# Performance work log

Measured on AMD Instinct MI355X. Metric: run time of the kernel, lower is better.

## Reference

```python
import jax, jax.numpy as jnp
import numpy as np
import math

B_, L_, D_, N_ = 8, 2048, 1024, 64


def _ln(x, g, b):
    m = jnp.mean(x, axis=-1, keepdims=True)
    v = jnp.mean((x - m) ** 2, axis=-1, keepdims=True)
    return (x - m) / jnp.sqrt(v + 1e-5) * g + b


def _ssm_kernel(A, Bp, Cp, Dp, L):
    # diagonal SSM: lambda = exp(diag(A)); k[l] = C diag(lambda)^l B + D  -> shape (L,)
    a = jnp.diagonal(A)                                   # (N,)
    powers = jnp.exp(jnp.arange(L)[:, None] * a[None, :])  # (L, N) = lambda^l
    return powers @ (Bp[:, 0] * Cp[0]) + Dp[0]             # (L,)


def _causal_conv(h, k):
    # y[:, t, :] = sum_{j<=t} k[j] * h[:, t-j, :]  via zero-padded FFT (same math, O(L log L))
    L = h.shape[1]
    n = 2 * L
    Hf = jnp.fft.rfft(h, n=n, axis=1)
    Kf = jnp.fft.rfft(k, n=n)
    return jnp.fft.irfft(Hf * Kf[None, :, None], n=n, axis=1)[:, :L]


def _timestep_embedding(t, dim):
    half = dim // 2
    freqs = jnp.exp(jnp.arange(half) * (-math.log(10000.0) / (half - 1)))
    ang = t[:, None] * freqs[None, :]
    return jnp.concatenate([jnp.sin(ang), jnp.cos(ang)], axis=1)  # (B, dim)


def _conv1d(x, w, b):
    # x: (B, C, L), w: (O, I, 3) torch layout, padding=1
    y = jax.lax.conv_general_dilated(x, w, (1,), [(1, 1)],
                                     dimension_numbers=('NCH', 'OIH', 'NCH'))
    return y + b[None, :, None]


def setup_inputs():
    key = jax.random.key(0)
    ks = jax.random.split(key, 26)
    d = {}
    d['x'] = jax.random.normal(ks[0], (B_, L_, D_), jnp.float32)
    d['t'] = jax.random.uniform(ks[1], (B_,), jnp.float32) * 1000.0
    d['beta1'] = jax.random.uniform(ks[2], (1,), jnp.float32)
    d['beta2'] = jax.random.uniform(ks[3], (1,), jnp.float32)
    sc = 1.0 / math.sqrt(D_)
    d['Wi'] = jax.random.normal(ks[4], (D_, D_), jnp.float32) * sc
    d['bi'] = jnp.zeros((D_,), jnp.float32)
    d['Wo'] = jax.random.normal(ks[5], (D_, D_), jnp.float32) * sc
    d['bo'] = jnp.zeros((D_,), jnp.float32)
    d['w1'] = jax.random.normal(ks[6], (D_, D_, 3), jnp.float32) * 0.02
    d['bc1'] = jnp.zeros((D_,), jnp.float32)
    d['w2'] = jax.random.normal(ks[7], (D_, D_, 3), jnp.float32) * 0.02
    d['bc2'] = jnp.zeros((D_,), jnp.float32)
    d['g1'] = jnp.ones((D_,), jnp.float32)
    d['b1'] = jnp.zeros((D_,), jnp.float32)
    d['g2'] = jnp.ones((D_,), jnp.float32)
    d['b2'] = jnp.zeros((D_,), jnp.float32)
    # SSM params (std 0.001 on A keeps exp(l*a) bounded for l up to L)
    d['Af'] = jax.random.normal(ks[8], (N_, N_), jnp.float32) * 0.001
    d['Bf'] = jax.random.normal(ks[9], (N_, 1), jnp.float32) * 0.01
    d['Cf'] = jax.random.normal(ks[10], (1, N_), jnp.float32) * 0.01
    d['Df'] = jax.random.normal(ks[11], (1,), jnp.float32) * 0.01
    d['Ab'] = jax.random.normal(ks[12], (N_, N_), jnp.float32) * 0.001
    d['Bb'] = jax.random.normal(ks[13], (N_, 1), jnp.float32) * 0.01
    d['Cb'] = jax.random.normal(ks[14], (1, N_), jnp.float32) * 0.01
    d['Db'] = jax.random.normal(ks[15], (1,), jnp.float32) * 0.01
    return d


def reference(x, t, beta1, beta2, Wi, bi, Wo, bo, w1, bc1, w2, bc2,
              g1, b1, g2, b2, Af, Bf, Cf, Df, Ab, Bb, Cb, Db):
    Bsz, L, D = x.shape
    h = x @ Wi + bi
    h = _ln(h, g1, b1)
    # local conv branch
    hT = jnp.transpose(h, (0, 2, 1))                 # (B, D, L)
    co = jax.nn.silu(_conv1d(hT, w1, bc1))
    co = _conv1d(co, w2, bc2)
    conv_out = jnp.transpose(co, (0, 2, 1))          # (B, L, D)
    # bidirectional SSM global convolutions
    kf = _ssm_kernel(Af, Bf, Cf, Df, L)
    h_fwd = _causal_conv(h, kf)
    kb = _ssm_kernel(Ab, Bb, Cb, Db, L)
    h_bwd = jnp.flip(_causal_conv(jnp.flip(h, axis=1), kb), axis=1)
    # timestep-conditioned mixing
    noise_scale = jax.nn.sigmoid(_timestep_embedding(t, D))[:, None, :]  # (B,1,D)
    h = h_fwd * (beta1[0] * noise_scale) + h_bwd * (beta2[0] * noise_scale) + conv_out
    h = h @ Wo + bo
    h = _ln(h, g2, b2)
    return x + h
```

## Files before the change

kernel.cpp:

```cpp
#include <hip/hip_runtime.h>

#define Bq 8
#define Lq 2048
#define Dq 1024
#define LPq 2050

typedef unsigned short u16;
typedef __attribute__((ext_vector_type(8))) short bf16x8;
typedef __attribute__((ext_vector_type(4))) float f32x4;

__device__ __forceinline__ u16 f2bf(float f) {
  unsigned u = __float_as_uint(f);
  u += 0x7FFFu + ((u >> 16) & 1u);
  return (u16)(u >> 16);
}
__device__ __forceinline__ float bf2f(u16 s) {
  return __uint_as_float(((unsigned)s) << 16);
}
__device__ __forceinline__ void gld16(const u16* g, u16* l) {
  __builtin_amdgcn_global_load_lds((const __attribute__((address_space(1))) void*)g,
                                   (__attribute__((address_space(3))) void*)l, 16, 0, 0);
}


__global__ __launch_bounds__(256) void prep_small(
    const float* __restrict__ t,
    const float* __restrict__ Af, const float* __restrict__ Bf, const float* __restrict__ Cf, const float* __restrict__ Df,
    const float* __restrict__ Ab, const float* __restrict__ Bb, const float* __restrict__ Cb, const float* __restrict__ Db,
    float* __restrict__ kf, float* __restrict__ kb,
    float* __restrict__ ns,
    u16* __restrict__ hpad, u16* __restrict__ copad) {
  int tid = blockIdx.x * 256 + threadIdx.x;
  if (blockIdx.x < 8) {
    int l = tid;
    float sf = Df[0], sb = Db[0];
    for (int n = 0; n < 64; n++) {
      sf += __expf((float)l * Af[n * 64 + n]) * (Bf[n] * Cf[n]);
      sb += __expf((float)l * Ab[n * 64 + n]) * (Bb[n] * Cb[n]);
    }
    kf[l] = sf; kb[l] = sb;
  } else if (blockIdx.x < 40) {
    int i = tid - 2048;
    int b = i >> 10, d = i & 1023;
    float tb = t[b];
    float e;
    if (d < 512) {
      float f = __expf((float)d * (-logf(10000.f) / 511.f));
      e = sinf(tb * f);
    } else {
      float f = __expf((float)(d - 512) * (-logf(10000.f) / 511.f));
      e = cosf(tb * f);
    }
    ns[i] = 1.f / (1.f + __expf(-e));
  } else {
    int i = tid - 10240;
    if (i < 32768) {
      int d = i & 1023;
      int j = i >> 10;
      int arr = j & 1, r = (j >> 1) & 1, b = j >> 2;
      size_t off = (size_t)b * LPq * Dq + (r ? (size_t)(LPq - 1) * Dq : 0) + d;
      if (arr == 0) hpad[off] = 0;
      else          copad[off] = 0;
    }
  }
}

__global__ __launch_bounds__(256) void mega_prep(
    const float* __restrict__ x, u16* __restrict__ xb,
    const float* __restrict__ Wi, u16* __restrict__ wit,
    const float* __restrict__ Wo, u16* __restrict__ wot,
    const float* __restrict__ w1, u16* __restrict__ w1t,
    const float* __restrict__ w2, u16* __restrict__ w2t,
    const float* __restrict__ kf, const float* __restrict__ kb,
    const float* __restrict__ be1, const float* __restrict__ be2,
    u16* __restrict__ Tm) {
  int bid = blockIdx.x, tid = threadIdx.x;
  if (bid < 8192) {
    size_t i = ((size_t)bid * 256 + tid) * 8;
    float4 a = *(const float4*)(x + i);
    float4 b = *(const float4*)(x + i + 4);
    u16 o[8] = {f2bf(a.x), f2bf(a.y), f2bf(a.z), f2bf(a.w),
                f2bf(b.x), f2bf(b.y), f2bf(b.z), f2bf(b.w)};
    *(bf16x8*)(xb + i) = *(const bf16x8*)o;
  } else if (bid < 8704) {
    __shared__ float tile[64][65];
    const float* W = (bid < 8448) ? Wi : Wo;
    u16* Wt = (bid < 8448) ? wit : wot;
    int b2 = (bid < 8448) ? bid - 8192 : bid - 8448;
    int bx = b2 & 15, by = b2 >> 4;
    int tx = tid & 63, tw = tid >> 6;
    for (int r = tw; r < 64; r += 4)
      tile[r][tx] = W[(size_t)(by * 64 + r) * 1024 + bx * 64 + tx];
    __syncthreads();
    for (int r = tw; r < 64; r += 4)
      Wt[(size_t)(bx * 64 + r) * 1024 + by * 64 + tx] = f2bf(tile[tx][r]);
  } else if (bid < 14848) {
    const float* w = (bid < 11776) ? w1 : w2;
    u16* Wt = (bid < 11776) ? w1t : w2t;
    int vb = (bid < 11776) ? bid - 8704 : bid - 11776;
    int base = (vb * 256 + tid) * 4;
    int o = base / 3072, rem = base % 3072;
    int dt = rem >> 10, i0 = rem & 1023;
    const float* src = w + (size_t)o * 3072 + dt;
    ushort4 v;
    v.x = f2bf(src[(i0 + 0) * 3]);
    v.y = f2bf(src[(i0 + 1) * 3]);
    v.z = f2bf(src[(i0 + 2) * 3]);
    v.w = f2bf(src[(i0 + 3) * 3]);
    *(ushort4*)(Wt + base) = v;
  } else {
    int idx = (bid - 14848) * 256 + tid;
    int tr = idx >> 9, j0 = (idx & 511) * 4;
    float b1v = be1[0], b2v = be2[0];
    ushort4 v;
#pragma unroll
    for (int q = 0; q < 4; q++) {
      int j = j0 + q;
      float vv = 0.f;
      if (tr >= j) vv += b1v * kf[tr - j];
      if (j >= tr) vv += b2v * kb[j - tr];
      ((u16*)&v)[q] = f2bf(vv);
    }
    *(ushort4*)(Tm + (size_t)tr * 2048 + j0) = v;
  }
}

__global__ __launch_bounds__(256) void trans_h(const u16* __restrict__ hpad, u16* __restrict__ ht) {
  __shared__ u16 tile[64][66];
  int b = blockIdx.z;
  int lt = blockIdx.x * 64, dt = blockIdx.y * 64;
  int tx = threadIdx.x & 15, ty = threadIdx.x >> 4;
  const u16* src = hpad + (size_t)b * LPq * Dq + (size_t)(lt + 1 + ty) * Dq + dt + tx * 4;
#pragma unroll
  for (int i = 0; i < 4; i++) {
    int r = ty + i * 16;
    ushort4 v = *(const ushort4*)(src + (size_t)i * 16 * Dq);
    tile[tx * 4 + 0][r] = v.x;
    tile[tx * 4 + 1][r] = v.y;
    tile[tx * 4 + 2][r] = v.z;
    tile[tx * 4 + 3][r] = v.w;
  }
  __syncthreads();
#pragma unroll
  for (int i = 0; i < 4; i++) {
    int d = ty + i * 16;
    ushort4 v;
    v.x = tile[d][tx * 4 + 0];
    v.y = tile[d][tx * 4 + 1];
    v.z = tile[d][tx * 4 + 2];
    v.w = tile[d][tx * 4 + 3];
    *(ushort4*)(ht + ((size_t)b * Dq + dt + d) * Lq + lt + tx * 4) = v;
  }
}


__global__ __launch_bounds__(256) void ln1_k(const u16* __restrict__ h0, u16* __restrict__ hpad,
                                             const float* __restrict__ g, const float* __restrict__ be) {
  int w = threadIdx.x >> 6, lane = threadIdx.x & 63;
  int r = blockIdx.x * 4 + w;
  int d0 = lane * 16;
  const u16* hp = h0 + (size_t)r * 1024 + d0;
  bf16x8 va = *(const bf16x8*)hp;
  bf16x8 vb = *(const bf16x8*)(hp + 8);
  float v[16];
#pragma unroll
  for (int i = 0; i < 8; i++) { v[i] = bf2f((u16)va[i]); v[8 + i] = bf2f((u16)vb[i]); }
  float s = 0.f, q = 0.f;
#pragma unroll
  for (int i = 0; i < 16; i++) { s += v[i]; q += v[i] * v[i]; }
#pragma unroll
  for (int o = 32; o > 0; o >>= 1) { s += __shfl_xor(s, o); q += __shfl_xor(q, o); }
  float mean = s * (1.f / 1024.f);
  float rstd = rsqrtf(q * (1.f / 1024.f) - mean * mean + 1e-5f);
  const float4* g4 = (const float4*)(g + d0);
  const float4* b4 = (const float4*)(be + d0);
  u16 o16[16];
#pragma unroll
  for (int i = 0; i < 4; i++) {
    float4 gv = g4[i], bv = b4[i];
    o16[i * 4 + 0] = f2bf((v[i * 4 + 0] - mean) * rstd * gv.x + bv.x);
    o16[i * 4 + 1] = f2bf((v[i * 4 + 1] - mean) * rstd * gv.y + bv.y);
    o16[i * 4 + 2] = f2bf((v[i * 4 + 2] - mean) * rstd * gv.z + bv.z);
    o16[i * 4 + 3] = f2bf((v[i * 4 + 3] - mean) * rstd * gv.w + bv.w);
  }
  int b_ = r >> 11, l = r & 2047;
  u16* dst = hpad + ((size_t)b_ * LPq + l + 1) * Dq + d0;
  *(bf16x8*)dst = *(const bf16x8*)o16;
  *(bf16x8*)(dst + 8) = *(const bf16x8*)(o16 + 8);
}

__global__ __launch_bounds__(256) void ln2_k(const u16* __restrict__ hp, const float* __restrict__ x,
                                             const float* __restrict__ g, const float* __restrict__ be,
                                             float* __restrict__ out) {
  int w = threadIdx.x >> 6, lane = threadIdx.x & 63;
  size_t r = (size_t)blockIdx.x * 4 + w;
  int d0 = lane * 16;
  size_t base = r * 1024 + d0;
  const u16* h = hp + base;
  bf16x8 va = *(const bf16x8*)h;
  bf16x8 vb = *(const bf16x8*)(h + 8);
  float v[16];
#pragma unroll
  for (int i = 0; i < 8; i++) { v[i] = bf2f((u16)va[i]); v[8 + i] = bf2f((u16)vb[i]); }
  float s = 0.f, q = 0.f;
#pragma unroll
  for (int i = 0; i < 16; i++) { s += v[i]; q += v[i] * v[i]; }
#pragma unroll
  for (int o = 32; o > 0; o >>= 1) { s += __shfl_xor(s, o); q += __shfl_xor(q, o); }
  float mean = s * (1.f / 1024.f);
  float rstd = rsqrtf(q * (1.f / 1024.f) - mean * mean + 1e-5f);
  const float4* g4 = (const float4*)(g + d0);
  const float4* b4 = (const float4*)(be + d0);
  const float4* x4 = (const float4*)(x + base);
  float4* o4 = (float4*)(out + base);
#pragma unroll
  for (int i = 0; i < 4; i++) {
    float4 gv = g4[i], bv = b4[i], xv = x4[i];
    float4 o;
    o.x = xv.x + (v[i * 4 + 0] - mean) * rstd * gv.x + bv.x;
    o.y = xv.y + (v[i * 4 + 1] - mean) * rstd * gv.y + bv.y;
    o.z = xv.z + (v[i * 4 + 2] - mean) * rstd * gv.z + bv.z;
    o.w = xv.w + (v[i * 4 + 3] - mean) * rstd * gv.w + bv.w;
    o4[i] = o;
  }
}

__device__ __forceinline__ void gemm_core(const u16* __restrict__ Ab, int lda,
                                          const u16* __restrict__ Bb, int ldb,
                                          int ks, int NS, u16* lds,
                                          f32x4 (&acc)[8][4]) {
  const int t = threadIdx.x;
  const int lane = t & 63, w = t >> 6;
  const int g = w >> 2, j = w & 3;
  const int p1 = t >> 3;
  const int c1 = (t & 7) ^ (p1 & 7);
  const int row1 = (p1 << 1) | (c1 >> 2), f1 = c1 & 3;
  const int q2 = t + 512;
  const int p2 = q2 >> 3;
  const int c2 = (q2 & 7) ^ (p2 & 7);
  const int row2 = (p2 << 1) | (c2 >> 2), f2 = c2 & 3;
  const int aoff1 = row1 * lda + f1 * 8;
  const int aoff2 = row2 * lda + f2 * 8;
  const int boff1 = row1 * ldb + f1 * 8;
  const int boff2 = row2 * ldb + f2 * 8;
  u16* wA1 = lds + t * 8;
  u16* wA2 = lds + 4096 + t * 8;
  u16* wB1 = lds + 8192 + t * 8;
  u16* wB2 = lds + 12288 + t * 8;
  const int frow = lane & 15, fkc = lane >> 4;
  const int arow = g * 128 + frow;
  const int pa = arow >> 1, ca = ((arow & 1) << 2) | fkc;
  const int abase = pa * 64 + ((ca ^ (pa & 7)) << 3);
  const int brow = j * 64 + frow;
  const int pb = brow >> 1, cb = ((brow & 1) << 2) | fkc;
  const int bbase = 8192 + pb * 64 + ((cb ^ (pb & 7)) << 3);

#define STAGE_A(s_) { int sl_ = ((s_) & 3) * 16384; const u16* g_ = Ab + ks + (s_) * 32; \
    gld16(g_ + aoff1, wA1 + sl_); gld16(g_ + aoff2, wA2 + sl_); }
#define STAGE_B(s_) { int sl_ = ((s_) & 3) * 16384; const u16* g_ = Bb + ks + (s_) * 32; \
    gld16(g_ + boff1, wB1 + sl_); gld16(g_ + boff2, wB2 + sl_); }

  STAGE_A(0); STAGE_B(0);
  STAGE_A(1); STAGE_B(1);
  STAGE_A(2); STAGE_B(2);

  for (int s = 0; s < NS; s++) {
    const u16* sl = lds + (s & 3) * 16384;
    if (s <= NS - 3)      { asm volatile("s_waitcnt vmcnt(8)" ::: "memory"); }
    else if (s == NS - 2) { asm volatile("s_waitcnt vmcnt(4)" ::: "memory"); }
    else                  { asm volatile("s_waitcnt vmcnt(0)" ::: "memory"); }
    asm volatile("s_barrier" ::: "memory");
    if (s + 3 < NS) STAGE_A(s + 3);
    bf16x8 bq[4], af[4];
#pragma unroll
    for (int nf = 0; nf < 4; nf++) bq[nf] = *(const bf16x8*)(sl + bbase + nf * 512);
#pragma unroll
    for (int mf = 0; mf < 4; mf++) af[mf] = *(const bf16x8*)(sl + abase + mf * 512);
    __builtin_amdgcn_s_setprio(1);
#pragma unroll
    for (int mf = 0; mf < 4; mf++)
#pragma unroll
      for (int nf = 0; nf < 4; nf++)
        acc[mf][nf] = __builtin_amdgcn_mfma_f32_16x16x32_bf16(af[mf], bq[nf], acc[mf][nf], 0, 0, 0);
    __builtin_amdgcn_s_setprio(0);
    if (s + 3 < NS) STAGE_B(s + 3);
#pragma unroll
    for (int mf = 0; mf < 4; mf++) af[mf] = *(const bf16x8*)(sl + abase + 2048 + mf * 512);
    __builtin_amdgcn_s_setprio(1);
#pragma unroll
    for (int mf = 0; mf < 4; mf++)
#pragma unroll
      for (int nf = 0; nf < 4; nf++)
        acc[4 + mf][nf] = __builtin_amdgcn_mfma_f32_16x16x32_bf16(af[mf], bq[nf], acc[4 + mf][nf], 0, 0, 0);
    __builtin_amdgcn_s_setprio(0);
  }
#undef STAGE_A
#undef STAGE_B
}

template <int MODE>
__global__ __launch_bounds__(512, 2) void gemm8(
    const u16* __restrict__ A, int lda, long abstr,
    const u16* __restrict__ Bw, int ldb,
    u16* __restrict__ Out, long obstr,
    const float* __restrict__ bias, int K, int nbm) {
  __shared__ __align__(16) u16 lds[65536];
  int mb = blockIdx.x % nbm, nb = blockIdx.x / nbm;
  int m0 = mb * 256, n0 = nb * 256;
  int batch = m0 >> 11, r0 = m0 & 2047;
  const u16* Ab = A + (size_t)batch * abstr + (size_t)r0 * lda;
  const u16* Bb = Bw + (size_t)n0 * ldb;
  f32x4 acc[8][4] = {};
  gemm_core(Ab, lda, Bb, ldb, 0, K >> 5, lds, acc);
  int lane = threadIdx.x & 63, w = threadIdx.x >> 6;
  int g = w >> 2, j = w & 3;
  int frow = lane & 15;
  u16* ob = Out + (size_t)batch * obstr;
#pragma unroll
  for (int mf = 0; mf < 8; mf++) {
    int row = r0 + g * 128 + mf * 16 + ((lane >> 4) << 2);
#pragma unroll
    for (int nf = 0; nf < 4; nf++) {
      int col = n0 + j * 64 + nf * 16 + frow;
      float bv = bias[col];
      size_t base = (size_t)row * 1024 + col;
      f32x4 a = acc[mf][nf];
#pragma unroll
      for (int i = 0; i < 4; i++) {
        float v = a[i] + bv;
        if (MODE == 1) v = v / (1.f + __expf(-v));
        if (MODE == 2) v += bf2f(ob[base + (size_t)i * 1024]);
        ob[base + (size_t)i * 1024] = f2bf(v);
      }
    }
  }
}

__global__ __launch_bounds__(512, 2) void ssm8(
    const u16* __restrict__ Tm, const u16* __restrict__ Ht,
    const float* __restrict__ ns, u16* __restrict__ out) {
  __shared__ __align__(16) u16 lds[65536];
  int mb = blockIdx.x & 7, nb = blockIdx.x >> 3;
  int m0 = mb * 256, n0 = nb * 256;
  const u16* Ab = Tm + (size_t)m0 * 2048;
  const u16* Bb = Ht + (size_t)n0 * 2048;
  f32x4 acc[8][4] = {};
  gemm_core(Ab, 2048, Bb, 2048, 0, 64, lds, acc);
  int lane = threadIdx.x & 63, w = threadIdx.x >> 6;
  int g = w >> 2, j = w & 3;
  int frow = lane & 15;
#pragma unroll
  for (int mf = 0; mf < 8; mf++) {
    int row = m0 + g * 128 + mf * 16 + ((lane >> 4) << 2);
#pragma unroll
    for (int nf = 0; nf < 4; nf++) {
      int col = n0 + j * 64 + nf * 16 + frow;
      int b = col >> 10, d = col & 1023;
      float cv = ns[col];
      u16* op = out + ((size_t)b * Lq + row) * 1024 + d;
      f32x4 a = acc[mf][nf];
#pragma unroll
      for (int i = 0; i < 4; i++)
        op[(size_t)i * 1024] = f2bf(a[i] * cv);
    }
  }
}


extern "C" void kernel_launch(void* const* d_in, const int* in_sizes, int n_in,
                              void* d_out, int out_size, void* d_ws, size_t ws_size,
                              hipStream_t stream) {
  const float* x   = (const float*)d_in[0];
  const float* tt  = (const float*)d_in[1];
  const float* be1 = (const float*)d_in[2];
  const float* be2 = (const float*)d_in[3];
  const float* Wi  = (const float*)d_in[4];
  const float* bi  = (const float*)d_in[5];
  const float* Wo  = (const float*)d_in[6];
  const float* bo  = (const float*)d_in[7];
  const float* w1  = (const float*)d_in[8];
  const float* bc1 = (const float*)d_in[9];
  const float* w2  = (const float*)d_in[10];
  const float* bc2 = (const float*)d_in[11];
  const float* g1  = (const float*)d_in[12];
  const float* b1  = (const float*)d_in[13];
  const float* g2  = (const float*)d_in[14];
  const float* b2  = (const float*)d_in[15];
  const float* Af  = (const float*)d_in[16];
  const float* Bf  = (const float*)d_in[17];
  const float* Cf  = (const float*)d_in[18];
  const float* Df  = (const float*)d_in[19];
  const float* Ab  = (const float*)d_in[20];
  const float* Bb  = (const float*)d_in[21];
  const float* Cb  = (const float*)d_in[22];
  const float* Db  = (const float*)d_in[23];

  char* p = (char*)d_ws;
  constexpr size_t SZ_h0   = (size_t)16384 * 1024 * 2;
  constexpr size_t SZ_hpad = (size_t)Bq * LPq * Dq * 2;
  constexpr size_t SZ_ht   = (size_t)Bq * Dq * Lq * 2;
  constexpr size_t SZ_hmix = (size_t)16384 * 1024 * 2;
  constexpr size_t SZ_T    = (size_t)2048 * 2048 * 2;
  constexpr size_t SZ_wt   = (size_t)1024 * 1024 * 2;
  constexpr size_t SZ_w3t  = (size_t)1024 * 3072 * 2;

  size_t off = 0;
  u16* h0    = (u16*)(p + off); off += SZ_h0;
  u16* hpad  = (u16*)(p + off); off += SZ_hpad;
  u16* ht    = (u16*)(p + off); off += SZ_ht;
  u16* copad = (u16*)(p + off); off += SZ_hpad;
  u16* hmixF = (u16*)(p + off); off += SZ_hmix;
  u16* Tmat  = (u16*)(p + off); off += SZ_T;
  u16* wit   = (u16*)(p + off); off += SZ_wt;
  u16* wot   = (u16*)(p + off); off += SZ_wt;
  u16* w1t   = (u16*)(p + off); off += SZ_w3t;
  u16* w2t   = (u16*)(p + off); off += SZ_w3t;
  float* kf  = (float*)(p + off); off += 8192;
  float* kb  = (float*)(p + off); off += 8192;
  float* nsb = (float*)(p + off); off += 32768;
  u16* xb    = hmixF;

  const long BSTR = (long)2048 * 1024;
  const long PSTR = (long)LPq * 1024;

  prep_small<<<dim3(168), dim3(256), 0, stream>>>(tt, Af, Bf, Cf, Df,
                                                  Ab, Bb, Cb, Db, kf, kb, nsb, hpad, copad);
  mega_prep<<<dim3(18944), dim3(256), 0, stream>>>(x, xb, Wi, wit, Wo, wot,
                                                   w1, w1t, w2, w2t, kf, kb, be1, be2, Tmat);

  gemm8<0><<<dim3(256), dim3(512), 0, stream>>>(xb, 1024, BSTR, wit, 1024, h0, BSTR, bi, 1024, 64);
  ln1_k<<<dim3(4096), dim3(256), 0, stream>>>(h0, hpad, g1, b1);
  trans_h<<<dim3(32, 16, 8), dim3(256), 0, stream>>>(hpad, ht);
  gemm8<1><<<dim3(256), dim3(512), 0, stream>>>(hpad, 1024, PSTR, w1t, 3072, copad + 1024, PSTR, bc1, 3072, 64);
  ssm8<<<dim3(256), dim3(512), 0, stream>>>(Tmat, ht, nsb, hmixF);
  gemm8<2><<<dim3(256), dim3(512), 0, stream>>>(copad, 1024, PSTR, w2t, 3072, hmixF, BSTR, bc2, 3072, 64);
  gemm8<0><<<dim3(256), dim3(512), 0, stream>>>(hmixF, 1024, BSTR, wot, 1024, h0, BSTR, bo, 1024, 64);
  ln2_k<<<dim3(4096), dim3(256), 0, stream>>>(h0, x, g2, b2, (float*)d_out);
}
```

Baseline: 446.6 us.

## Switch GEMM core to 32x32x16 MFMA and merge conv1 and SSM GEMMs into one launch

The shared GEMM core now uses 32x32x16 bf16 MFMA tiles instead of 16x16x32. That means fewer instructions and fewer LDS fragment reads per unit of output, with the LDS addressing and epilogue row/column mapping rewritten to match. The conv1 GEMM (with SiLU) and the SSM Toeplitz GEMM are independent, so they are fused into a single 512-block kernel. This lets both fill the GPU together and removes one launch and its tail. The cost is an epilogue layout that must match the 32x32 accumulator ordering, and register use stays the same.

After: 478.0 us. +7.0%, slower.

```diff
diff --git a/kernel.cpp b/kernel.cpp
--- a/kernel.cpp
+++ b/kernel.cpp
@@ -7,7 +7,7 @@
 
 typedef unsigned short u16;
 typedef __attribute__((ext_vector_type(8))) short bf16x8;
-typedef __attribute__((ext_vector_type(4))) float f32x4;
+typedef __attribute__((ext_vector_type(16))) float f32x16;
 
 __device__ __forceinline__ u16 f2bf(float f) {
   unsigned u = __float_as_uint(f);
@@ -228,7 +228,7 @@
 __device__ __forceinline__ void gemm_core(const u16* __restrict__ Ab, int lda,
                                           const u16* __restrict__ Bb, int ldb,
                                           int ks, int NS, u16* lds,
-                                          f32x4 (&acc)[8][4]) {
+                                          f32x16 (&acc)[4][2]) {
   const int t = threadIdx.x;
   const int lane = t & 63, w = t >> 6;
   const int g = w >> 2, j = w & 3;
@@ -247,13 +247,24 @@
   u16* wA2 = lds + 4096 + t * 8;
   u16* wB1 = lds + 8192 + t * 8;
   u16* wB2 = lds + 12288 + t * 8;
-  const int frow = lane & 15, fkc = lane >> 4;
-  const int arow = g * 128 + frow;
-  const int pa = arow >> 1, ca = ((arow & 1) << 2) | fkc;
-  const int abase = pa * 64 + ((ca ^ (pa & 7)) << 3);
-  const int brow = j * 64 + frow;
-  const int pb = brow >> 1, cb = ((brow & 1) << 2) | fkc;
-  const int bbase = 8192 + pb * 64 + ((cb ^ (pb & 7)) << 3);
+  const int r32 = lane & 31, kh = lane >> 5;
+  int aadr[4][2], badr[2][2];
+#pragma unroll
+  for (int mf = 0; mf < 4; mf++)
+#pragma unroll
+    for (int kk = 0; kk < 2; kk++) {
+      int r = g * 128 + mf * 32 + r32;
+      int p = r >> 1, c = ((r & 1) << 2) | (kk * 2 + kh);
+      aadr[mf][kk] = p * 64 + ((c ^ (p & 7)) << 3);
+    }
+#pragma unroll
+  for (int nf = 0; nf < 2; nf++)
+#pragma unroll
+    for (int kk = 0; kk < 2; kk++) {
+      int r = j * 64 + nf * 32 + r32;
+      int p = r >> 1, c = ((r & 1) << 2) | (kk * 2 + kh);
+      badr[nf][kk] = 8192 + p * 64 + ((c ^ (p & 7)) << 3);
+    }
 
 #define STAGE_A(s_) { int sl_ = ((s_) & 3) * 16384; const u16* g_ = Ab + ks + (s_) * 32; \
     gld16(g_ + aoff1, wA1 + sl_); gld16(g_ + aoff2, wA2 + sl_); }
@@ -271,27 +282,30 @@
     else                  { asm volatile("s_waitcnt vmcnt(0)" ::: "memory"); }
     asm volatile("s_barrier" ::: "memory");
     if (s + 3 < NS) STAGE_A(s + 3);
-    bf16x8 bq[4], af[4];
-#pragma unroll
-    for (int nf = 0; nf < 4; nf++) bq[nf] = *(const bf16x8*)(sl + bbase + nf * 512);
-#pragma unroll
-    for (int mf = 0; mf < 4; mf++) af[mf] = *(const bf16x8*)(sl + abase + mf * 512);
+    bf16x8 b0[2], b1[2], a0[4], a1[4];
+#pragma unroll
+    for (int nf = 0; nf < 2; nf++) {
+      b0[nf] = *(const bf16x8*)(sl + badr[nf][0]);
+      b1[nf] = *(const bf16x8*)(sl + badr[nf][1]);
+    }
+#pragma unroll
+    for (int mf = 0; mf < 4; mf++) a0[mf] = *(const bf16x8*)(sl + aadr[mf][0]);
     __builtin_amdgcn_s_setprio(1);
 #pragma unroll
     for (int mf = 0; mf < 4; mf++)
 #pragma unroll
-      for (int nf = 0; nf < 4; nf++)
-        acc[mf][nf] = __builtin_amdgcn_mfma_f32_16x16x32_bf16(af[mf], bq[nf], acc[mf][nf], 0, 0, 0);
+      for (int nf = 0; nf < 2; nf++)
+        acc[mf][nf] = __builtin_amdgcn_mfma_f32_32x32x16_bf16(a0[mf], b0[nf], acc[mf][nf], 0, 0, 0);
     __builtin_amdgcn_s_setprio(0);
     if (s + 3 < NS) STAGE_B(s + 3);
 #pragma unroll
-    for (int mf = 0; mf < 4; mf++) af[mf] = *(const bf16x8*)(sl + abase + 2048 + mf * 512);
+    for (int mf = 0; mf < 4; mf++) a1[mf] = *(const bf16x8*)(sl + aadr[mf][1]);
     __builtin_amdgcn_s_setprio(1);
 #pragma unroll
     for (int mf = 0; mf < 4; mf++)
 #pragma unroll
-      for (int nf = 0; nf < 4; nf++)
-        acc[4 + mf][nf] = __builtin_amdgcn_mfma_f32_16x16x32_bf16(af[mf], bq[nf], acc[4 + mf][nf], 0, 0, 0);
+      for (int nf = 0; nf < 2; nf++)
+        acc[mf][nf] = __builtin_amdgcn_mfma_f32_32x32x16_bf16(a1[mf], b1[nf], acc[mf][nf], 0, 0, 0);
     __builtin_amdgcn_s_setprio(0);
   }
 #undef STAGE_A
@@ -310,58 +324,100 @@
   int batch = m0 >> 11, r0 = m0 & 2047;
   const u16* Ab = A + (size_t)batch * abstr + (size_t)r0 * lda;
   const u16* Bb = Bw + (size_t)n0 * ldb;
-  f32x4 acc[8][4] = {};
+  f32x16 acc[4][2] = {};
   gemm_core(Ab, lda, Bb, ldb, 0, K >> 5, lds, acc);
   int lane = threadIdx.x & 63, w = threadIdx.x >> 6;
   int g = w >> 2, j = w & 3;
-  int frow = lane & 15;
+  int r32 = lane & 31, kh = lane >> 5;
   u16* ob = Out + (size_t)batch * obstr;
 #pragma unroll
-  for (int mf = 0; mf < 8; mf++) {
-    int row = r0 + g * 128 + mf * 16 + ((lane >> 4) << 2);
-#pragma unroll
-    for (int nf = 0; nf < 4; nf++) {
-      int col = n0 + j * 64 + nf * 16 + frow;
+  for (int mf = 0; mf < 4; mf++) {
+#pragma unroll
+    for (int nf = 0; nf < 2; nf++) {
+      int col = n0 + j * 64 + nf * 32 + r32;
       float bv = bias[col];
-      size_t base = (size_t)row * 1024 + col;
-      f32x4 a = acc[mf][nf];
-#pragma unroll
-      for (int i = 0; i < 4; i++) {
-        float v = a[i] + bv;
-        if (MODE == 1) v = v / (1.f + __expf(-v));
-        if (MODE == 2) v += bf2f(ob[base + (size_t)i * 1024]);
-        ob[base + (size_t)i * 1024] = f2bf(v);
+      f32x16 a = acc[mf][nf];
+#pragma unroll
+      for (int q = 0; q < 4; q++) {
+        int row = r0 + g * 128 + mf * 32 + q * 8 + 4 * kh;
+        u16* op = ob + (size_t)row * 1024 + col;
+#pragma unroll
+        for (int i = 0; i < 4; i++) {
+          float v = a[q * 4 + i] + bv;
+          if (MODE == 1) v = v / (1.f + __expf(-v));
+          if (MODE == 2) v += bf2f(op[(size_t)i * 1024]);
+          op[(size_t)i * 1024] = f2bf(v);
+        }
       }
     }
   }
 }
 
-__global__ __launch_bounds__(512, 2) void ssm8(
+__global__ __launch_bounds__(512, 2) void mix8(
+    const u16* __restrict__ hpad, const u16* __restrict__ w1t,
+    u16* __restrict__ co, const float* __restrict__ bc1,
     const u16* __restrict__ Tm, const u16* __restrict__ Ht,
-    const float* __restrict__ ns, u16* __restrict__ out) {
+    const float* __restrict__ ns, u16* __restrict__ hmix) {
   __shared__ __align__(16) u16 lds[65536];
-  int mb = blockIdx.x & 7, nb = blockIdx.x >> 3;
-  int m0 = mb * 256, n0 = nb * 256;
-  const u16* Ab = Tm + (size_t)m0 * 2048;
-  const u16* Bb = Ht + (size_t)n0 * 2048;
-  f32x4 acc[8][4] = {};
-  gemm_core(Ab, 2048, Bb, 2048, 0, 64, lds, acc);
+  const long PSTR = (long)LPq * 1024;
+  int id = blockIdx.x;
   int lane = threadIdx.x & 63, w = threadIdx.x >> 6;
   int g = w >> 2, j = w & 3;
-  int frow = lane & 15;
-#pragma unroll
-  for (int mf = 0; mf < 8; mf++) {
-    int row = m0 + g * 128 + mf * 16 + ((lane >> 4) << 2);
-#pragma unroll
-    for (int nf = 0; nf < 4; nf++) {
-      int col = n0 + j * 64 + nf * 16 + frow;
-      int b = col >> 10, d = col & 1023;
-      float cv = ns[col];
-      u16* op = out + ((size_t)b * Lq + row) * 1024 + d;
-      f32x4 a = acc[mf][nf];
-#pragma unroll
-      for (int i = 0; i < 4; i++)
-        op[(size_t)i * 1024] = f2bf(a[i] * cv);
+  int r32 = lane & 31, kh = lane >> 5;
+  if (id < 256) {
+    int mb = id & 63, nb = id >> 6;
+    int m0 = mb * 256, n0 = nb * 256;
+    int batch = m0 >> 11, r0 = m0 & 2047;
+    const u16* Ab = hpad + (size_t)batch * PSTR + (size_t)r0 * 1024;
+    const u16* Bb = w1t + (size_t)n0 * 3072;
+    f32x16 acc[4][2] = {};
+    gemm_core(Ab, 1024, Bb, 3072, 0, 96, lds, acc);
+    u16* ob = co + (size_t)batch * PSTR;
+#pragma unroll
+    for (int mf = 0; mf < 4; mf++) {
+#pragma unroll
+      for (int nf = 0; nf < 2; nf++) {
+        int col = n0 + j * 64 + nf * 32 + r32;
+        float bv = bc1[col];
+        f32x16 a = acc[mf][nf];
+#pragma unroll
+        for (int q = 0; q < 4; q++) {
+          int row = r0 + g * 128 + mf * 32 + q * 8 + 4 * kh;
+          u16* op = ob + (size_t)row * 1024 + col;
+#pragma unroll
+          for (int i = 0; i < 4; i++) {
+            float v = a[q * 4 + i] + bv;
+            v = v / (1.f + __expf(-v));
+            op[(size_t)i * 1024] = f2bf(v);
+          }
+        }
+      }
+    }
+  } else {
+    int r = id - 256;
+    int mb = r & 7, nb = r >> 3;
+    int m0 = mb * 256, n0 = nb * 256;
+    const u16* Ab = Tm + (size_t)m0 * 2048;
+    const u16* Bb = Ht + (size_t)n0 * 2048;
+    f32x16 acc[4][2] = {};
+    gemm_core(Ab, 2048, Bb, 2048, 0, 64, lds, acc);
+#pragma unroll
+    for (int mf = 0; mf < 4; mf++) {
+#pragma unroll
+      for (int nf = 0; nf < 2; nf++) {
+        int col = n0 + j * 64 + nf * 32 + r32;
+        int b = col >> 10, d = col & 1023;
+        float cv = ns[col];
+        f32x16 a = acc[mf][nf];
+#pragma unroll
+        for (int q = 0; q < 4; q++) {
+          int row = m0 + g * 128 + mf * 32 + q * 8 + 4 * kh;
+          u16* op = hmix + ((size_t)b * Lq + row) * 1024 + d;
+#pragma unroll
+          for (int i = 0; i < 4; i++)
+            op[(size_t)i * 1024] = f2bf(a[q * 4 + i] * cv);
+        }
+      }
     }
   }
 }
@@ -431,8 +487,8 @@
   gemm8<0><<<dim3(256), dim3(512), 0, stream>>>(xb, 1024, BSTR, wit, 1024, h0, BSTR, bi, 1024, 64);
   ln1_k<<<dim3(4096), dim3(256), 0, stream>>>(h0, hpad, g1, b1);
   trans_h<<<dim3(32, 16, 8), dim3(256), 0, stream>>>(hpad, ht);
-  gemm8<1><<<dim3(256), dim3(512), 0, stream>>>(hpad, 1024, PSTR, w1t, 3072, copad + 1024, PSTR, bc1, 3072, 64);
-  ssm8<<<dim3(256), dim3(512), 0, stream>>>(Tmat, ht, nsb, hmixF);
+  mix8<<<dim3(512), dim3(512), 0, stream>>>(hpad, w1t, copad + 1024, bc1,
+                                            Tmat, ht, nsb, hmixF);
   gemm8<2><<<dim3(256), dim3(512), 0, stream>>>(copad, 1024, PSTR, w2t, 3072, hmixF, BSTR, bc2, 3072, 64);
   gemm8<0><<<dim3(256), dim3(512), 0, stream>>>(hmixF, 1024, BSTR, wot, 1024, h0, BSTR, bo, 1024, 64);
   ln2_k<<<dim3(4096), dim3(256), 0, stream>>>(h0, x, g2, b2, (float*)d_out);
```

## Use K=64 double-buffered GEMM tiles and merge conv1 and SSM GEMMs into one launch

Applied to the files above, without the earlier changes.

The GEMM core now stages 64-wide K slices into two LDS buffers instead of 32-wide slices into a four-deep ring, so each stage issues four async loads per operand and waits on vmcnt(0) before the barrier. The first conv GEMM and the SSM Toeplitz GEMM, which are independent, are merged into a single 512-block launch. This lowers launch overhead and fills the GPU with both workloads at once. The cost is a shallower prefetch pipeline (one stage ahead with a full wait), which may expose more memory latency.

Result: faster. 407.3 us (-8.8%).

```diff
diff --git a/kernel.cpp b/kernel.cpp
--- a/kernel.cpp
+++ b/kernel.cpp
@@ -227,55 +227,52 @@
 
 __device__ __forceinline__ void gemm_core(const u16* __restrict__ Ab, int lda,
                                           const u16* __restrict__ Bb, int ldb,
-                                          int ks, int NS, u16* lds,
+                                          int NS, u16* lds,
                                           f32x4 (&acc)[8][4]) {
   const int t = threadIdx.x;
   const int lane = t & 63, w = t >> 6;
   const int g = w >> 2, j = w & 3;
-  const int p1 = t >> 3;
-  const int c1 = (t & 7) ^ (p1 & 7);
-  const int row1 = (p1 << 1) | (c1 >> 2), f1 = c1 & 3;
-  const int q2 = t + 512;
-  const int p2 = q2 >> 3;
-  const int c2 = (q2 & 7) ^ (p2 & 7);
-  const int row2 = (p2 << 1) | (c2 >> 2), f2 = c2 & 3;
-  const int aoff1 = row1 * lda + f1 * 8;
-  const int aoff2 = row2 * lda + f2 * 8;
-  const int boff1 = row1 * ldb + f1 * 8;
-  const int boff2 = row2 * ldb + f2 * 8;
-  u16* wA1 = lds + t * 8;
-  u16* wA2 = lds + 4096 + t * 8;
-  u16* wB1 = lds + 8192 + t * 8;
-  u16* wB2 = lds + 12288 + t * 8;
-  const int frow = lane & 15, fkc = lane >> 4;
-  const int arow = g * 128 + frow;
-  const int pa = arow >> 1, ca = ((arow & 1) << 2) | fkc;
-  const int abase = pa * 64 + ((ca ^ (pa & 7)) << 3);
-  const int brow = j * 64 + frow;
-  const int pb = brow >> 1, cb = ((brow & 1) << 2) | fkc;
-  const int bbase = 8192 + pb * 64 + ((cb ^ (pb & 7)) << 3);
-
-#define STAGE_A(s_) { int sl_ = ((s_) & 3) * 16384; const u16* g_ = Ab + ks + (s_) * 32; \
-    gld16(g_ + aoff1, wA1 + sl_); gld16(g_ + aoff2, wA2 + sl_); }
-#define STAGE_B(s_) { int sl_ = ((s_) & 3) * 16384; const u16* g_ = Bb + ks + (s_) * 32; \
-    gld16(g_ + boff1, wB1 + sl_); gld16(g_ + boff2, wB2 + sl_); }
+  int aoff[4], boff[4];
+#pragma unroll
+  for (int q = 0; q < 4; q++) {
+    int c = t + q * 512;
+    int row = c >> 3;
+    int slot = (c & 7) ^ (row & 7);
+    aoff[q] = row * lda + slot * 8;
+    boff[q] = row * ldb + slot * 8;
+  }
+  const int frow = lane & 15, f = lane >> 4;
+  int aadr[8], badr[4];
+#pragma unroll
+  for (int mf = 0; mf < 8; mf++) {
+    int row = g * 128 + mf * 16 + frow;
+    aadr[mf] = row * 64 + ((f ^ (row & 7)) << 3);
+  }
+#pragma unroll
+  for (int nf = 0; nf < 4; nf++) {
+    int row = j * 64 + nf * 16 + frow;
+    badr[nf] = 16384 + row * 64 + ((f ^ (row & 7)) << 3);
+  }
+
+#define STAGE_A(s_) { const u16* g_ = Ab + (s_) * 64; u16* l_ = lds + ((s_) & 1) * 32768; \
+    gld16(g_ + aoff[0], l_ + t * 8);            gld16(g_ + aoff[1], l_ + (t + 512) * 8); \
+    gld16(g_ + aoff[2], l_ + (t + 1024) * 8);   gld16(g_ + aoff[3], l_ + (t + 1536) * 8); }
+#define STAGE_B(s_) { const u16* g_ = Bb + (s_) * 64; u16* l_ = lds + ((s_) & 1) * 32768 + 16384; \
+    gld16(g_ + boff[0], l_ + t * 8);            gld16(g_ + boff[1], l_ + (t + 512) * 8); \
+    gld16(g_ + boff[2], l_ + (t + 1024) * 8);   gld16(g_ + boff[3], l_ + (t + 1536) * 8); }
 
   STAGE_A(0); STAGE_B(0);
-  STAGE_A(1); STAGE_B(1);
-  STAGE_A(2); STAGE_B(2);
 
   for (int s = 0; s < NS; s++) {
-    const u16* sl = lds + (s & 3) * 16384;
-    if (s <= NS - 3)      { asm volatile("s_waitcnt vmcnt(8)" ::: "memory"); }
-    else if (s == NS - 2) { asm volatile("s_waitcnt vmcnt(4)" ::: "memory"); }
-    else                  { asm volatile("s_waitcnt vmcnt(0)" ::: "memory"); }
+    const u16* sl = lds + (s & 1) * 32768;
+    asm volatile("s_waitcnt vmcnt(0)" ::: "memory");
     asm volatile("s_barrier" ::: "memory");
-    if (s + 3 < NS) STAGE_A(s + 3);
+    if (s + 1 < NS) STAGE_A(s + 1);
     bf16x8 bq[4], af[4];
 #pragma unroll
-    for (int nf = 0; nf < 4; nf++) bq[nf] = *(const bf16x8*)(sl + bbase + nf * 512);
-#pragma unroll
-    for (int mf = 0; mf < 4; mf++) af[mf] = *(const bf16x8*)(sl + abase + mf * 512);
+    for (int nf = 0; nf < 4; nf++) bq[nf] = *(const bf16x8*)(sl + badr[nf]);
+#pragma unroll
+    for (int mf = 0; mf < 4; mf++) af[mf] = *(const bf16x8*)(sl + aadr[mf]);
     __builtin_amdgcn_s_setprio(1);
 #pragma unroll
     for (int mf = 0; mf < 4; mf++)
@@ -283,9 +280,29 @@
       for (int nf = 0; nf < 4; nf++)
         acc[mf][nf] = __builtin_amdgcn_mfma_f32_16x16x32_bf16(af[mf], bq[nf], acc[mf][nf], 0, 0, 0);
     __builtin_amdgcn_s_setprio(0);
-    if (s + 3 < NS) STAGE_B(s + 3);
-#pragma unroll
-    for (int mf = 0; mf < 4; mf++) af[mf] = *(const bf16x8*)(sl + abase + 2048 + mf * 512);
+    if (s + 1 < NS) STAGE_B(s + 1);
+#pragma unroll
+    for (int mf = 0; mf < 4; mf++) af[mf] = *(const bf16x8*)(sl + aadr[4 + mf]);
+    __builtin_amdgcn_s_setprio(1);
+#pragma unroll
+    for (int mf = 0; mf < 4; mf++)
+#pragma unroll
+      for (int nf = 0; nf < 4; nf++)
+        acc[4 + mf][nf] = __builtin_amdgcn_mfma_f32_16x16x32_bf16(af[mf], bq[nf], acc[4 + mf][nf], 0, 0, 0);
+    __builtin_amdgcn_s_setprio(0);
+#pragma unroll
+    for (int nf = 0; nf < 4; nf++) bq[nf] = *(const bf16x8*)(sl + (badr[nf] ^ 32));
+#pragma unroll
+    for (int mf = 0; mf < 4; mf++) af[mf] = *(const bf16x8*)(sl + (aadr[mf] ^ 32));
+    __builtin_amdgcn_s_setprio(1);
+#pragma unroll
+    for (int mf = 0; mf < 4; mf++)
+#pragma unroll
+      for (int nf = 0; nf < 4; nf++)
+        acc[mf][nf] = __builtin_amdgcn_mfma_f32_16x16x32_bf16(af[mf], bq[nf], acc[mf][nf], 0, 0, 0);
+    __builtin_amdgcn_s_setprio(0);
+#pragma unroll
+    for (int mf = 0; mf < 4; mf++) af[mf] = *(const bf16x8*)(sl + (aadr[4 + mf] ^ 32));
     __builtin_amdgcn_s_setprio(1);
 #pragma unroll
     for (int mf = 0; mf < 4; mf++)
@@ -311,7 +328,7 @@
   const u16* Ab = A + (size_t)batch * abstr + (size_t)r0 * lda;
   const u16* Bb = Bw + (size_t)n0 * ldb;
   f32x4 acc[8][4] = {};
-  gemm_core(Ab, lda, Bb, ldb, 0, K >> 5, lds, acc);
+  gemm_core(Ab, lda, Bb, ldb, K >> 6, lds, acc);
   int lane = threadIdx.x & 63, w = threadIdx.x >> 6;
   int g = w >> 2, j = w & 3;
   int frow = lane & 15;
@@ -336,32 +353,65 @@
   }
 }
 
-__global__ __launch_bounds__(512, 2) void ssm8(
+__global__ __launch_bounds__(512, 2) void mix8(
+    const u16* __restrict__ hpad, const u16* __restrict__ w1t,
+    u16* __restrict__ co, const float* __restrict__ bc1,
     const u16* __restrict__ Tm, const u16* __restrict__ Ht,
-    const float* __restrict__ ns, u16* __restrict__ out) {
+    const float* __restrict__ ns, u16* __restrict__ hmix) {
   __shared__ __align__(16) u16 lds[65536];
-  int mb = blockIdx.x & 7, nb = blockIdx.x >> 3;
-  int m0 = mb * 256, n0 = nb * 256;
-  const u16* Ab = Tm + (size_t)m0 * 2048;
-  const u16* Bb = Ht + (size_t)n0 * 2048;
-  f32x4 acc[8][4] = {};
-  gemm_core(Ab, 2048, Bb, 2048, 0, 64, lds, acc);
+  const long PSTR = (long)LPq * 1024;
+  int id = blockIdx.x;
   int lane = threadIdx.x & 63, w = threadIdx.x >> 6;
   int g = w >> 2, j = w & 3;
   int frow = lane & 15;
-#pragma unroll
-  for (int mf = 0; mf < 8; mf++) {
-    int row = m0 + g * 128 + mf * 16 + ((lane >> 4) << 2);
-#pragma unroll
-    for (int nf = 0; nf < 4; nf++) {
-      int col = n0 + j * 64 + nf * 16 + frow;
-      int b = col >> 10, d = col & 1023;
-      float cv = ns[col];
-      u16* op = out + ((size_t)b * Lq + row) * 1024 + d;
-      f32x4 a = acc[mf][nf];
-#pragma unroll
-      for (int i = 0; i < 4; i++)
-        op[(size_t)i * 1024] = f2bf(a[i] * cv);
+  if (id < 256) {
+    int mb = id & 63, nb = id >> 6;
+    int m0 = mb * 256, n0 = nb * 256;
+    int batch = m0 >> 11, r0 = m0 & 2047;
+    const u16* Ab = hpad + (size_t)batch * PSTR + (size_t)r0 * 1024;
+    const u16* Bb = w1t + (size_t)n0 * 3072;
+    f32x4 acc[8][4] = {};
+    gemm_core(Ab, 1024, Bb, 3072, 48, lds, acc);
+    u16* ob = co + (size_t)batch * PSTR;
+#pragma unroll
+    for (int mf = 0; mf < 8; mf++) {
+      int row = r0 + g * 128 + mf * 16 + ((lane >> 4) << 2);
+#pragma unroll
+      for (int nf = 0; nf < 4; nf++) {
+        int col = n0 + j * 64 + nf * 16 + frow;
+        float bv = bc1[col];
+        size_t base = (size_t)row * 1024 + col;
+        f32x4 a = acc[mf][nf];
+#pragma unroll
+        for (int i = 0; i < 4; i++) {
+          float v = a[i] + bv;
+          v = v / (1.f + __expf(-v));
+          ob[base + (size_t)i * 1024] = f2bf(v);
+        }
+      }
+    }
+  } else {
+    int r = id - 256;
+    int mb = r & 7, nb = r >> 3;
+    int m0 = mb * 256, n0 = nb * 256;
+    const u16* Ab = Tm + (size_t)m0 * 2048;
+    const u16* Bb = Ht + (size_t)n0 * 2048;
+    f32x4 acc[8][4] = {};
+    gemm_core(Ab, 2048, Bb, 2048, 32, lds, acc);
+#pragma unroll
+    for (int mf = 0; mf < 8; mf++) {
+      int row = m0 + g * 128 + mf * 16 + ((lane >> 4) << 2);
+#pragma unroll
+      for (int nf = 0; nf < 4; nf++) {
+        int col = n0 + j * 64 + nf * 16 + frow;
+        int b = col >> 10, d = col & 1023;
+        float cv = ns[col];
+        u16* op = hmix + ((size_t)b * Lq + row) * 1024 + d;
+        f32x4 a = acc[mf][nf];
+#pragma unroll
+        for (int i = 0; i < 4; i++)
+          op[(size_t)i * 1024] = f2bf(a[i] * cv);
+      }
     }
   }
 }
@@ -431,8 +481,8 @@
   gemm8<0><<<dim3(256), dim3(512), 0, stream>>>(xb, 1024, BSTR, wit, 1024, h0, BSTR, bi, 1024, 64);
   ln1_k<<<dim3(4096), dim3(256), 0, stream>>>(h0, hpad, g1, b1);
   trans_h<<<dim3(32, 16, 8), dim3(256), 0, stream>>>(hpad, ht);
-  gemm8<1><<<dim3(256), dim3(512), 0, stream>>>(hpad, 1024, PSTR, w1t, 3072, copad + 1024, PSTR, bc1, 3072, 64);
-  ssm8<<<dim3(256), dim3(512), 0, stream>>>(Tmat, ht, nsb, hmixF);
+  mix8<<<dim3(512), dim3(512), 0, stream>>>(hpad, w1t, copad + 1024, bc1,
+                                            Tmat, ht, nsb, hmixF);
   gemm8<2><<<dim3(256), dim3(512), 0, stream>>>(copad, 1024, PSTR, w2t, 3072, hmixF, BSTR, bc2, 3072, 64);
   gemm8<0><<<dim3(256), dim3(512), 0, stream>>>(hmixF, 1024, BSTR, wot, 1024, h0, BSTR, bo, 1024, 64);
   ln2_k<<<dim3(4096), dim3(256), 0, stream>>>(h0, x, g2, b2, (float*)d_out);
```
